# Kernel tuning notes

Measured on AMD Instinct MI355X. Metric: run time of the kernel, lower is better.

The kernel has to match this reference:

```python
import jax, jax.numpy as jnp
import numpy as np

H = 4       # N_head
C = 32      # c_hidden
CZ = 128    # c_z
N = 256
B = 1
EPS = 1e-5


def setup_inputs() -> dict:
    key = jax.random.key(0)
    ks = jax.random.split(key, 8)
    hc = H * C
    return {
        "z": jax.random.normal(ks[0], (B, N, N, CZ), dtype=jnp.float32),
        "ln_scale": jnp.ones((CZ,), dtype=jnp.float32),
        "ln_bias": jnp.zeros((CZ,), dtype=jnp.float32),
        "Wq": jax.random.normal(ks[1], (CZ, hc), dtype=jnp.float32) * 0.02,
        "Wk": jax.random.normal(ks[2], (CZ, hc), dtype=jnp.float32) * 0.02,
        "Wv": jax.random.normal(ks[3], (CZ, hc), dtype=jnp.float32) * 0.02,
        "Wb": jax.random.normal(ks[4], (CZ, H), dtype=jnp.float32) * 0.02,
        "Wg": jax.random.normal(ks[5], (CZ, hc), dtype=jnp.float32) * 0.02,
        "Wo": jax.random.normal(ks[6], (hc, CZ), dtype=jnp.float32) * 0.02,
    }


def reference(z, ln_scale, ln_bias, Wq, Wk, Wv, Wb, Wg, Wo):
    b, n = z.shape[0], z.shape[1]
    # LayerNorm over c_z
    mu = jnp.mean(z, axis=-1, keepdims=True)
    var = jnp.mean(jnp.square(z - mu), axis=-1, keepdims=True)
    zn = (z - mu) * jax.lax.rsqrt(var + EPS) * ln_scale + ln_bias
    # projections -> [B, N, N, H, C]
    q = (zn @ Wq).reshape(b, n, n, H, C)
    k = (zn @ Wk).reshape(b, n, n, H, C)
    v = (zn @ Wv).reshape(b, n, n, H, C)
    bias = zn @ Wb                                  # [B, N, N, H]
    g = jax.nn.sigmoid(zn @ Wg).reshape(b, n, n, H, C)
    # attention around starting node i: query at (i,j), keys/values at (i,k)
    scores = jnp.einsum('bijhd,bikhd->bijkh', q, k) * (1.0 / C ** 0.5)
    scores = scores + bias[:, None, :, :, :]        # bias[b, j, k, h]
    a = jax.nn.softmax(scores, axis=-2)             # softmax over k
    o = jnp.einsum('bijkh,bikhd->bijhd', a, v)      # [B, N, N, H, C]
    o = (g * o).reshape(b, n, n, H * C)
    return o @ Wo
```

## Files before the change

kernel.cpp:

```cpp
#include <hip/hip_runtime.h>
#include <math.h>

#define NN 256
#define CZ 128
#define NH 4
#define CH 32
#define HC 128
#define NPIX (NN*NN)
#define L2E   1.4426950408889634f
#define SCALE2 (0.17677669529663687f * 1.4426950408889634f)

typedef __attribute__((ext_vector_type(8))) short bf16x8;
typedef __attribute__((ext_vector_type(4))) float fx4;
typedef __attribute__((ext_vector_type(4))) unsigned u32x4;

__device__ __forceinline__ unsigned pack_hl(float x) {
    unsigned b  = __builtin_bit_cast(unsigned, x);
    unsigned hb = b & 0xFFFF0000u;
    float r = x - __builtin_bit_cast(float, hb);
    return hb | (__builtin_bit_cast(unsigned, r) >> 16);
}
__device__ __forceinline__ void load_split8(const float* p, bf16x8& h, bf16x8& l) {
    float4 x0 = *(const float4*)p;
    float4 x1 = *(const float4*)(p + 4);
    float xs[8] = {x0.x, x0.y, x0.z, x0.w, x1.x, x1.y, x1.z, x1.w};
    #pragma unroll
    for (int j = 0; j < 8; ++j) {
        unsigned b  = __builtin_bit_cast(unsigned, xs[j]);
        unsigned hb = b & 0xFFFF0000u;
        float r = xs[j] - __builtin_bit_cast(float, hb);
        h[j] = (short)(hb >> 16);
        l[j] = (short)(__builtin_bit_cast(unsigned, r) >> 16);
    }
}
__device__ __forceinline__ void deint_raw(u32x4 e0, u32x4 e1, bf16x8& h, bf16x8& l) {
    unsigned es[8] = {e0[0], e0[1], e0[2], e0[3], e1[0], e1[1], e1[2], e1[3]};
    unsigned hw[4], lw[4];
    #pragma unroll
    for (int j = 0; j < 4; ++j) {
        unsigned a = es[2 * j], b = es[2 * j + 1];
        hw[j] = (a >> 16) | (b & 0xFFFF0000u);
        lw[j] = (a & 0x0000FFFFu) | (b << 16);
    }
    h = __builtin_bit_cast(bf16x8, u32x4{hw[0], hw[1], hw[2], hw[3]});
    l = __builtin_bit_cast(bf16x8, u32x4{lw[0], lw[1], lw[2], lw[3]});
}
__device__ __forceinline__ void deint8(const unsigned* p, bf16x8& h, bf16x8& l) {
    u32x4 e0 = *(const u32x4*)p;
    u32x4 e1 = *(const u32x4*)(p + 4);
    deint_raw(e0, e1, h, l);
}

__device__ __forceinline__ void qtrans(unsigned &x, unsigned &y) {
#if __has_builtin(__builtin_amdgcn_permlane32_swap) && __has_builtin(__builtin_amdgcn_permlane16_swap)
    {
        auto r = __builtin_amdgcn_permlane32_swap(x, y, false, false);
        x = r[0]; y = r[1];
    }
    {
        auto r = __builtin_amdgcn_permlane16_swap(x, y, false, false);
        x = r[0]; y = r[1];
    }
#else
    asm("v_permlane32_swap_b32 %0, %1\n\t"
        "v_permlane16_swap_b32 %0, %1" : "+v"(x), "+v"(y));
#endif
}

__global__ __launch_bounds__(256) void pack_w_kernel(
    const float* __restrict__ Wq, const float* __restrict__ Wk,
    const float* __restrict__ Wv, const float* __restrict__ Wg,
    const float* __restrict__ Wo, bf16x8* __restrict__ pk)
{
    int id  = blockIdx.x * 256 + threadIdx.x;
    int mid = id >> 11;
    int e   = id & 2047;
    const float* W = (mid == 0) ? Wq : (mid == 1) ? Wk : (mid == 2) ? Wv : (mid == 3) ? Wg : Wo;
    int quad = e & 3, n = (e >> 2) & 127, ks = e >> 9;
    int k0 = ks * 32 + quad * 8;
    bf16x8 h, l;
    #pragma unroll
    for (int j = 0; j < 8; ++j) {
        float x = W[(size_t)(k0 + j) * 128 + n];
        unsigned b  = __builtin_bit_cast(unsigned, x);
        unsigned hb = b & 0xFFFF0000u;
        float r = x - __builtin_bit_cast(float, hb);
        h[j] = (short)(hb >> 16);
        l[j] = (short)(__builtin_bit_cast(unsigned, r) >> 16);
    }
    pk[(size_t)mid * 4096 + e]        = h;
    pk[(size_t)mid * 4096 + 2048 + e] = l;
}

__global__ __launch_bounds__(256) void ln_proj_kernel(
    const float* __restrict__ z, const float* __restrict__ ls, const float* __restrict__ lb,
    const float* __restrict__ Wb, const bf16x8* __restrict__ pk,
    unsigned* __restrict__ q_pk, unsigned* __restrict__ k_pk, unsigned* __restrict__ v_pk,
    float* __restrict__ g_ws, float* __restrict__ bias_n)
{
    __shared__ float zsh[32][132];
    __shared__ float wbsh[512];

    const int t  = threadIdx.x;
    const int p0 = blockIdx.x * 32;
    const int i  = p0 >> 8;
    const int j0 = p0 & 255;

    wbsh[t]       = Wb[t];
    wbsh[t + 256] = Wb[t + 256];

    const int p = t >> 3, sub = t & 7;
    float4 zv[4];
    {
        const float4* zp = (const float4*)(z + (size_t)(p0 + p) * CZ + sub * 16);
        #pragma unroll
        for (int r = 0; r < 4; ++r) zv[r] = zp[r];
    }
    float s = 0.f, q = 0.f;
    #pragma unroll
    for (int r = 0; r < 4; ++r) {
        s += ((zv[r].x + zv[r].y) + (zv[r].z + zv[r].w));
        q += ((zv[r].x * zv[r].x + zv[r].y * zv[r].y)
            + (zv[r].z * zv[r].z + zv[r].w * zv[r].w));
    }
    #pragma unroll
    for (int m = 1; m <= 4; m <<= 1) {
        s += __shfl_xor(s, m, 64);
        q += __shfl_xor(q, m, 64);
    }
    {
        float mu  = s * (1.0f / 128.0f);
        float var = q * (1.0f / 128.0f) - mu * mu;
        float a   = var + 1e-5f;
        float r0  = rsqrtf(a);
        r0 = r0 * (1.5f - 0.5f * a * r0 * r0);
        #pragma unroll
        for (int r = 0; r < 4; ++r) {
            float4 s4 = ((const float4*)ls)[sub * 4 + r];
            float4 b4 = ((const float4*)lb)[sub * 4 + r];
            float4 v  = zv[r];
            v.x = (v.x - mu) * r0 * s4.x + b4.x;
            v.y = (v.y - mu) * r0 * s4.y + b4.y;
            v.z = (v.z - mu) * r0 * s4.z + b4.z;
            v.w = (v.w - mu) * r0 * s4.w + b4.w;
            *(float4*)&zsh[p][sub * 16 + r * 4] = v;
        }
    }
    __syncthreads();

    const int wv = t >> 6, lane = t & 63;
    const int lrow = lane & 15, quad = lane >> 4;
    const bf16x8* ph = pk + (size_t)wv * 4096;
    const bf16x8* pl = ph + 2048;

    fx4 acc[2][8];
    #pragma unroll
    for (int mr = 0; mr < 2; ++mr)
        #pragma unroll
        for (int nc = 0; nc < 8; ++nc)
            acc[mr][nc] = fx4{0.f, 0.f, 0.f, 0.f};

    #pragma unroll
    for (int ks = 0; ks < 4; ++ks) {
        bf16x8 ah[2], al[2];
        #pragma unroll
        for (int mr = 0; mr < 2; ++mr)
            load_split8(&zsh[mr * 16 + lrow][ks * 32 + quad * 8], ah[mr], al[mr]);
        #pragma unroll
        for (int nc = 0; nc < 8; ++nc) {
            int bi = (ks * 128 + nc * 16 + lrow) * 4 + quad;
            bf16x8 bh = ph[bi], bl = pl[bi];
            #pragma unroll
            for (int mr = 0; mr < 2; ++mr) {
                acc[mr][nc] = __builtin_amdgcn_mfma_f32_16x16x32_bf16(ah[mr], bl, acc[mr][nc], 0, 0, 0);
                acc[mr][nc] = __builtin_amdgcn_mfma_f32_16x16x32_bf16(al[mr], bh, acc[mr][nc], 0, 0, 0);
                acc[mr][nc] = __builtin_amdgcn_mfma_f32_16x16x32_bf16(ah[mr], bh, acc[mr][nc], 0, 0, 0);
            }
        }
    }

    #pragma unroll
    for (int mr = 0; mr < 2; ++mr) {
        #pragma unroll
        for (int nc = 0; nc < 8; ++nc) {
            int cg = nc * 16 + lrow;
            int h = cg >> 5, cc = cg & 31;
            int jl = mr * 16 + quad * 4;
            fx4 a = acc[mr][nc];
            if (wv == 0) {
                unsigned* qp = q_pk + ((size_t)(i * NH + h) * NN + j0 + jl) * CH + cc;
                #pragma unroll
                for (int r = 0; r < 4; ++r) qp[r * CH] = pack_hl(a[r]);
            } else if (wv == 1) {
                unsigned* kp = k_pk + ((size_t)(i * NH + h) * NN + j0 + jl) * CH + cc;
                #pragma unroll
                for (int r = 0; r < 4; ++r) kp[r * CH] = pack_hl(a[r]);
            } else if (wv == 2) {
                u32x4 e = {pack_hl(a[0]), pack_hl(a[1]), pack_hl(a[2]), pack_hl(a[3])};
                *(u32x4*)(v_pk + ((size_t)(i * NH + h) * CH + cc) * NN + j0 + jl) = e;
            } else {
                float* gp = g_ws + (size_t)(p0 + jl) * HC + cg;
                #pragma unroll
                for (int r = 0; r < 4; ++r) gp[r * HC] = 1.0f / (1.0f + __expf(-a[r]));
            }
        }
    }

    {
        int pair = t >> 1, half = t & 1;
        int hh = pair >> 5, pp = pair & 31;
        int d0 = half * 64;
        float b = 0.f;
        #pragma unroll 8
        for (int d = 0; d < 64; ++d)
            b = fmaf(zsh[pp][d0 + d], wbsh[(d0 + d) * 4 + hh], b);
        b += __shfl_xor(b, 1, 64);
        if (half == 0)
            bias_n[(size_t)hh * NPIX + (size_t)i * NN + j0 + pp] = b * L2E;
    }
}

__global__ __launch_bounds__(256) void attn_kernel(
    const unsigned* __restrict__ q_pk, const unsigned* __restrict__ k_pk,
    const unsigned* __restrict__ v_pk, const float* __restrict__ g_ws,
    const float* __restrict__ bias_n, float* __restrict__ go_ws)
{
    const int t = threadIdx.x;
    const int wv = t >> 6, lane = t & 63;
    const int lrow = lane & 15, quad = lane >> 4;
    const int h = blockIdx.x & 3, i = blockIdx.x >> 2;
    const int qb = wv * 64;

    const unsigned* qs = q_pk + (size_t)(i * NH + h) * NN * CH;
    const unsigned* ks = k_pk + (size_t)(i * NH + h) * NN * CH;
    const unsigned* vs = v_pk + (size_t)(i * NH + h) * CH * NN;
    const float*    bs = bias_n + (size_t)h * NPIX;

    bf16x8 qh[4], ql[4];
    #pragma unroll
    for (int nt = 0; nt < 4; ++nt)
        deint8(qs + (size_t)(qb + nt * 16 + lrow) * CH + quad * 8, qh[nt], ql[nt]);

    u32x4 krA[2], krB[2];
    #pragma unroll
    for (int mt = 0; mt < 2; ++mt) {
        const u32x4* kp = (const u32x4*)(ks + (size_t)(mt * 16 + lrow) * CH + quad * 8);
        krA[mt] = kp[0]; krB[mt] = kp[1];
    }

    fx4 oacc[2][4];
    #pragma unroll
    for (int ct = 0; ct < 2; ++ct)
        #pragma unroll
        for (int nt = 0; nt < 4; ++nt)
            oacc[ct][nt] = fx4{0.f, 0.f, 0.f, 0.f};
    float lsum[4] = {0.f, 0.f, 0.f, 0.f};

    for (int kb = 0; kb < NN; kb += 32) {
        u32x4 vrA[2], vrB[2];
        #pragma unroll
        for (int ct = 0; ct < 2; ++ct) {
            const u32x4* vp = (const u32x4*)(vs + (size_t)(ct * 16 + lrow) * NN + kb + quad * 8);
            vrA[ct] = vp[0]; vrB[ct] = vp[1];
        }
        float4 bv[4][2];
        #pragma unroll
        for (int nt = 0; nt < 4; ++nt)
            #pragma unroll
            for (int mt = 0; mt < 2; ++mt)
                bv[nt][mt] = *(const float4*)(bs + (size_t)(qb + nt * 16 + lrow) * NN
                                                 + kb + mt * 16 + quad * 4);
        const int kb2 = (kb + 32) & (NN - 1);
        u32x4 nkA[2], nkB[2];
        #pragma unroll
        for (int mt = 0; mt < 2; ++mt) {
            const u32x4* kp = (const u32x4*)(ks + (size_t)(kb2 + mt * 16 + lrow) * CH + quad * 8);
            nkA[mt] = kp[0]; nkB[mt] = kp[1];
        }

        bf16x8 kh[2], kl_[2];
        #pragma unroll
        for (int mt = 0; mt < 2; ++mt)
            deint_raw(krA[mt], krB[mt], kh[mt], kl_[mt]);

        fx4 sv[4][2];
        __builtin_amdgcn_s_setprio(1);
        #pragma unroll
        for (int nt = 0; nt < 4; ++nt) {
            #pragma unroll
            for (int mt = 0; mt < 2; ++mt) {
                fx4 s = fx4{0.f, 0.f, 0.f, 0.f};
                s = __builtin_amdgcn_mfma_f32_16x16x32_bf16(kh[mt],  ql[nt], s, 0, 0, 0);
                s = __builtin_amdgcn_mfma_f32_16x16x32_bf16(kl_[mt], qh[nt], s, 0, 0, 0);
                s = __builtin_amdgcn_mfma_f32_16x16x32_bf16(kh[mt],  qh[nt], s, 0, 0, 0);
                sv[nt][mt] = s;
            }
        }
        __builtin_amdgcn_s_setprio(0);

        bf16x8 vh[2], vl[2];
        #pragma unroll
        for (int ct = 0; ct < 2; ++ct)
            deint_raw(vrA[ct], vrB[ct], vh[ct], vl[ct]);

        unsigned w0h[4][2], w1h[4][2], w0l[4][2], w1l[4][2];
        #pragma unroll
        for (int nt = 0; nt < 4; ++nt) {
            #pragma unroll
            for (int mt = 0; mt < 2; ++mt) {
                fx4 s = sv[nt][mt];
                float4 b4 = bv[nt][mt];
                float e0 = exp2f(fmaf(s[0], SCALE2, b4.x));
                float e1 = exp2f(fmaf(s[1], SCALE2, b4.y));
                float e2 = exp2f(fmaf(s[2], SCALE2, b4.z));
                float e3 = exp2f(fmaf(s[3], SCALE2, b4.w));
                lsum[nt] += (e0 + e1) + (e2 + e3);

                unsigned b0 = __builtin_bit_cast(unsigned, e0);
                unsigned b1 = __builtin_bit_cast(unsigned, e1);
                unsigned b2 = __builtin_bit_cast(unsigned, e2);
                unsigned b3 = __builtin_bit_cast(unsigned, e3);
                unsigned h01 = (b0 >> 16) | (b1 & 0xFFFF0000u);
                unsigned h23 = (b2 >> 16) | (b3 & 0xFFFF0000u);
                float r0 = e0 - __builtin_bit_cast(float, b0 & 0xFFFF0000u);
                float r1 = e1 - __builtin_bit_cast(float, b1 & 0xFFFF0000u);
                float r2 = e2 - __builtin_bit_cast(float, b2 & 0xFFFF0000u);
                float r3 = e3 - __builtin_bit_cast(float, b3 & 0xFFFF0000u);
                unsigned l01 = (__builtin_bit_cast(unsigned, r0) >> 16)
                             | (__builtin_bit_cast(unsigned, r1) & 0xFFFF0000u);
                unsigned l23 = (__builtin_bit_cast(unsigned, r2) >> 16)
                             | (__builtin_bit_cast(unsigned, r3) & 0xFFFF0000u);
                w0h[nt][mt] = h01; w1h[nt][mt] = h23;
                w0l[nt][mt] = l01; w1l[nt][mt] = l23;
            }
        }

        #pragma unroll
        for (int nt = 0; nt < 4; ++nt) {
            qtrans(w0h[nt][0], w0h[nt][1]);
            qtrans(w1h[nt][0], w1h[nt][1]);
            qtrans(w0l[nt][0], w0l[nt][1]);
            qtrans(w1l[nt][0], w1l[nt][1]);
        }

        __builtin_amdgcn_s_setprio(1);
        #pragma unroll
        for (int nt = 0; nt < 4; ++nt) {
            bf16x8 pbh = __builtin_bit_cast(bf16x8,
                u32x4{w0h[nt][0], w1h[nt][0], w0h[nt][1], w1h[nt][1]});
            bf16x8 pbl = __builtin_bit_cast(bf16x8,
                u32x4{w0l[nt][0], w1l[nt][0], w0l[nt][1], w1l[nt][1]});
            #pragma unroll
            for (int ct = 0; ct < 2; ++ct) {
                oacc[ct][nt] = __builtin_amdgcn_mfma_f32_16x16x32_bf16(vh[ct], pbl, oacc[ct][nt], 0, 0, 0);
                oacc[ct][nt] = __builtin_amdgcn_mfma_f32_16x16x32_bf16(vl[ct], pbh, oacc[ct][nt], 0, 0, 0);
                oacc[ct][nt] = __builtin_amdgcn_mfma_f32_16x16x32_bf16(vh[ct], pbh, oacc[ct][nt], 0, 0, 0);
            }
        }
        __builtin_amdgcn_s_setprio(0);

        #pragma unroll
        for (int mt = 0; mt < 2; ++mt) { krA[mt] = nkA[mt]; krB[mt] = nkB[mt]; }
    }

    #pragma unroll
    for (int nt = 0; nt < 4; ++nt) {
        float s = lsum[nt];
        s += __shfl_xor(s, 16, 64);
        s += __shfl_xor(s, 32, 64);
        float inv = 1.0f / s;
        size_t pix = (size_t)i * NN + qb + nt * 16 + lrow;
        #pragma unroll
        for (int ct = 0; ct < 2; ++ct) {
            const float* gp = g_ws + pix * HC + h * CH + ct * 16 + quad * 4;
            float4 g4 = *(const float4*)gp;
            fx4 o = oacc[ct][nt];
            float4 r;
            r.x = g4.x * o[0] * inv;
            r.y = g4.y * o[1] * inv;
            r.z = g4.z * o[2] * inv;
            r.w = g4.w * o[3] * inv;
            *(float4*)(go_ws + pix * HC + h * CH + ct * 16 + quad * 4) = r;
        }
    }
}

__global__ __launch_bounds__(256) void outproj_kernel(
    const float* __restrict__ go_ws, const bf16x8* __restrict__ pk, float* __restrict__ out)
{
    const int t  = threadIdx.x;
    const int p0 = blockIdx.x * 64;
    const int wv = t >> 6, lane = t & 63;
    const int lrow = lane & 15, quad = lane >> 4;
    const bf16x8* ph = pk + (size_t)4 * 4096;
    const bf16x8* pl = ph + 2048;

    const float* grow = go_ws + (size_t)(p0 + wv * 16 + lrow) * HC + quad * 8;

    bf16x8 ah[4], al[4];
    #pragma unroll
    for (int ks = 0; ks < 4; ++ks)
        load_split8(grow + ks * 32, ah[ks], al[ks]);

    fx4 acc[8];
    #pragma unroll
    for (int nc = 0; nc < 8; ++nc) acc[nc] = fx4{0.f, 0.f, 0.f, 0.f};

    #pragma unroll
    for (int ks = 0; ks < 4; ++ks) {
        #pragma unroll
        for (int nc = 0; nc < 8; ++nc) {
            int bi = (ks * 128 + nc * 16 + lrow) * 4 + quad;
            bf16x8 bh = ph[bi], bl = pl[bi];
            acc[nc] = __builtin_amdgcn_mfma_f32_16x16x32_bf16(ah[ks], bl, acc[nc], 0, 0, 0);
            acc[nc] = __builtin_amdgcn_mfma_f32_16x16x32_bf16(al[ks], bh, acc[nc], 0, 0, 0);
            acc[nc] = __builtin_amdgcn_mfma_f32_16x16x32_bf16(ah[ks], bh, acc[nc], 0, 0, 0);
        }
    }

    #pragma unroll
    for (int nc = 0; nc < 8; ++nc) {
        #pragma unroll
        for (int r = 0; r < 4; ++r)
            out[(size_t)(p0 + wv * 16 + quad * 4 + r) * HC + nc * 16 + lrow] = acc[nc][r];
    }
}

extern "C" void kernel_launch(void* const* d_in, const int* in_sizes, int n_in,
                              void* d_out, int out_size, void* d_ws, size_t ws_size,
                              hipStream_t stream)
{
    const float* z  = (const float*)d_in[0];
    const float* ls = (const float*)d_in[1];
    const float* lb = (const float*)d_in[2];
    const float* Wq = (const float*)d_in[3];
    const float* Wk = (const float*)d_in[4];
    const float* Wv = (const float*)d_in[5];
    const float* Wb = (const float*)d_in[6];
    const float* Wg = (const float*)d_in[7];
    const float* Wo = (const float*)d_in[8];

    float* ws = (float*)d_ws;
    const size_t BIG = (size_t)NPIX * HC;
    unsigned* q_pk  = (unsigned*)ws;
    unsigned* k_pk  = (unsigned*)(ws + BIG);
    unsigned* v_pk  = (unsigned*)(ws + 2 * BIG);
    float* g_ws     = ws + 3 * BIG;
    float* go_ws    = ws + 4 * BIG;
    float* bias_n   = ws + 5 * BIG;
    bf16x8* pk      = (bf16x8*)(bias_n + (size_t)NH * NPIX);

    pack_w_kernel<<<40, 256, 0, stream>>>(Wq, Wk, Wv, Wg, Wo, pk);
    ln_proj_kernel<<<NPIX / 32, 256, 0, stream>>>(z, ls, lb, Wb, pk,
                                                  q_pk, k_pk, v_pk, g_ws, bias_n);
    attn_kernel<<<NN * NH, 256, 0, stream>>>(q_pk, k_pk, v_pk, g_ws, bias_n, go_ws);
    outproj_kernel<<<NPIX / 64, 256, 0, stream>>>(go_ws, pk, (float*)d_out);
}
```

Before: 246.2 us.

## Fuse output projection into attention kernel via shared-memory staging

Each attention block now covers 64 query rows for all four heads, one head per wave, instead of one head for all 256 rows. The gated attention output is staged in shared memory and multiplied by Wo inside the same kernel. This removes the separate out-projection launch and the full-size gated-output round trip through global memory. In exchange it adds a barrier, about 33 KB of LDS per block, and higher register pressure.

```diff
diff --git a/kernel.cpp b/kernel.cpp
--- a/kernel.cpp
+++ b/kernel.cpp
@@ -223,13 +223,17 @@
 __global__ __launch_bounds__(256) void attn_kernel(
     const unsigned* __restrict__ q_pk, const unsigned* __restrict__ k_pk,
     const unsigned* __restrict__ v_pk, const float* __restrict__ g_ws,
-    const float* __restrict__ bias_n, float* __restrict__ go_ws)
+    const float* __restrict__ bias_n, const bf16x8* __restrict__ pk,
+    float* __restrict__ out)
 {
+    __shared__ float gsh[64][132];
+
     const int t = threadIdx.x;
     const int wv = t >> 6, lane = t & 63;
     const int lrow = lane & 15, quad = lane >> 4;
-    const int h = blockIdx.x & 3, i = blockIdx.x >> 2;
-    const int qb = wv * 64;
+    const int jb = blockIdx.x & 3, i = blockIdx.x >> 2;
+    const int h = wv;
+    const int qb = jb * 64;
 
     const unsigned* qs = q_pk + (size_t)(i * NH + h) * NN * CH;
     const unsigned* ks = k_pk + (size_t)(i * NH + h) * NN * CH;
@@ -380,49 +384,43 @@
             r.y = g4.y * o[1] * inv;
             r.z = g4.z * o[2] * inv;
             r.w = g4.w * o[3] * inv;
-            *(float4*)(go_ws + pix * HC + h * CH + ct * 16 + quad * 4) = r;
-        }
-    }
-}
-
-__global__ __launch_bounds__(256) void outproj_kernel(
-    const float* __restrict__ go_ws, const bf16x8* __restrict__ pk, float* __restrict__ out)
-{
-    const int t  = threadIdx.x;
-    const int p0 = blockIdx.x * 64;
-    const int wv = t >> 6, lane = t & 63;
-    const int lrow = lane & 15, quad = lane >> 4;
-    const bf16x8* ph = pk + (size_t)4 * 4096;
-    const bf16x8* pl = ph + 2048;
-
-    const float* grow = go_ws + (size_t)(p0 + wv * 16 + lrow) * HC + quad * 8;
-
-    bf16x8 ah[4], al[4];
-    #pragma unroll
-    for (int ks = 0; ks < 4; ++ks)
-        load_split8(grow + ks * 32, ah[ks], al[ks]);
-
-    fx4 acc[8];
-    #pragma unroll
-    for (int nc = 0; nc < 8; ++nc) acc[nc] = fx4{0.f, 0.f, 0.f, 0.f};
-
-    #pragma unroll
-    for (int ks = 0; ks < 4; ++ks) {
+            *(float4*)&gsh[nt * 16 + lrow][h * CH + ct * 16 + quad * 4] = r;
+        }
+    }
+    __syncthreads();
+
+    {
+        const bf16x8* ph = pk + (size_t)4 * 4096;
+        const bf16x8* pl = ph + 2048;
+
+        bf16x8 ah[4], al[4];
+        #pragma unroll
+        for (int ksx = 0; ksx < 4; ++ksx)
+            load_split8(&gsh[wv * 16 + lrow][ksx * 32 + quad * 8], ah[ksx], al[ksx]);
+
+        fx4 acc[8];
+        #pragma unroll
+        for (int nc = 0; nc < 8; ++nc) acc[nc] = fx4{0.f, 0.f, 0.f, 0.f};
+
+        #pragma unroll
+        for (int ksx = 0; ksx < 4; ++ksx) {
+            #pragma unroll
+            for (int nc = 0; nc < 8; ++nc) {
+                int bi = (ksx * 128 + nc * 16 + lrow) * 4 + quad;
+                bf16x8 bh = ph[bi], bl = pl[bi];
+                acc[nc] = __builtin_amdgcn_mfma_f32_16x16x32_bf16(ah[ksx], bl, acc[nc], 0, 0, 0);
+                acc[nc] = __builtin_amdgcn_mfma_f32_16x16x32_bf16(al[ksx], bh, acc[nc], 0, 0, 0);
+                acc[nc] = __builtin_amdgcn_mfma_f32_16x16x32_bf16(ah[ksx], bh, acc[nc], 0, 0, 0);
+            }
+        }
+
+        const size_t prow = (size_t)i * NN + qb;
         #pragma unroll
         for (int nc = 0; nc < 8; ++nc) {
-            int bi = (ks * 128 + nc * 16 + lrow) * 4 + quad;
-            bf16x8 bh = ph[bi], bl = pl[bi];
-            acc[nc] = __builtin_amdgcn_mfma_f32_16x16x32_bf16(ah[ks], bl, acc[nc], 0, 0, 0);
-            acc[nc] = __builtin_amdgcn_mfma_f32_16x16x32_bf16(al[ks], bh, acc[nc], 0, 0, 0);
-            acc[nc] = __builtin_amdgcn_mfma_f32_16x16x32_bf16(ah[ks], bh, acc[nc], 0, 0, 0);
-        }
-    }
-
-    #pragma unroll
-    for (int nc = 0; nc < 8; ++nc) {
-        #pragma unroll
-        for (int r = 0; r < 4; ++r)
-            out[(size_t)(p0 + wv * 16 + quad * 4 + r) * HC + nc * 16 + lrow] = acc[nc][r];
+            #pragma unroll
+            for (int r = 0; r < 4; ++r)
+                out[(prow + wv * 16 + quad * 4 + r) * HC + nc * 16 + lrow] = acc[nc][r];
+        }
     }
 }
 
@@ -446,13 +444,12 @@
     unsigned* k_pk  = (unsigned*)(ws + BIG);
     unsigned* v_pk  = (unsigned*)(ws + 2 * BIG);
     float* g_ws     = ws + 3 * BIG;
-    float* go_ws    = ws + 4 * BIG;
     float* bias_n   = ws + 5 * BIG;
     bf16x8* pk      = (bf16x8*)(bias_n + (size_t)NH * NPIX);
 
     pack_w_kernel<<<40, 256, 0, stream>>>(Wq, Wk, Wv, Wg, Wo, pk);
     ln_proj_kernel<<<NPIX / 32, 256, 0, stream>>>(z, ls, lb, Wb, pk,
                                                   q_pk, k_pk, v_pk, g_ws, bias_n);
-    attn_kernel<<<NN * NH, 256, 0, stream>>>(q_pk, k_pk, v_pk, g_ws, bias_n, go_ws);
-    outproj_kernel<<<NPIX / 64, 256, 0, stream>>>(go_ws, pk, (float*)d_out);
-}
+    attn_kernel<<<NN * (NN / 64), 256, 0, stream>>>(q_pk, k_pk, v_pk, g_ws,
+                                                    bias_n, pk, (float*)d_out);
+}
```

Result: no change. 247.9 us (+0.7%).
